# Kernel optimization log

Hardware: AMD Instinct MI355X
Metric: run time of the kernel (lower is better)

The kernel has to match this reference:

```python
import jax, jax.numpy as jnp
import numpy as np

NEG_INF = -1e30


def setup_inputs() -> dict:
    key = jax.random.key(0)
    ks = jax.random.split(key, 7)
    N, C, B = 262144, 256, 8
    feats = jax.random.normal(ks[0], (N, C), dtype=jnp.float32)
    scores = jax.random.normal(ks[1], (N, 1), dtype=jnp.float32)
    w_reg = jax.random.normal(ks[2], (C, 6), dtype=jnp.float32) * 0.01
    w_cls = jax.random.normal(ks[3], (C, 18), dtype=jnp.float32) * 0.01
    b_cls = jax.random.normal(ks[4], (18,), dtype=jnp.float32) * 0.01
    scale = jnp.ones((1,), dtype=jnp.float32)
    batch_ids = jnp.sort(jax.random.randint(ks[5], (N,), 0, B, dtype=jnp.int32))
    return {"feats": feats, "scores": scores, "w_reg": w_reg, "w_cls": w_cls,
            "b_cls": b_cls, "scale": scale, "batch_ids": batch_ids,
            "n_batches": B, "pts_threshold": 8192}


def _prune_mask(scores, batch_ids, n_batches, k):
    # scores: [N,1]; per-batch top-k selection mask (torch.topk + scatter in original).
    s = jax.lax.stop_gradient(scores[:, 0])  # computed under no_grad in torch
    # [B, N]: score where point belongs to batch b, else -inf
    per_batch = jnp.where(batch_ids[None, :] == jnp.arange(n_batches, dtype=batch_ids.dtype)[:, None],
                          s[None, :], NEG_INF)
    kth = jax.lax.top_k(per_batch, k)[0][:, -1]  # [B] k-th largest per cloud
    return s >= kth[batch_ids]  # [N] bool


def reference(feats, scores, w_reg, w_cls, b_cls, scale, batch_ids, n_batches, pts_threshold):
    mask = _prune_mask(scores, batch_ids, n_batches, pts_threshold)
    x = feats * mask[:, None].astype(feats.dtype)  # MinkowskiPruning (fixed-shape: zero out)
    # FCAF3D heads: 1x1 sparse convs == per-point matmuls; reg goes through Scale + exp.
    bbox_pred = jnp.exp(scale[0] * (x @ w_reg))          # [N, 6]
    cls_score = x @ w_cls + b_cls                         # [N, 18]
    return jnp.concatenate([bbox_pred, cls_score], axis=-1)  # [N, 24]
```

## Files before the change

### kernel.cpp

```cpp
#include <hip/hip_runtime.h>
#include <hip/hip_bf16.h>

typedef unsigned int u32;
typedef unsigned short u16;
typedef unsigned long long u64;

#define NBINS 65536
#define MAXB 8

__device__ __forceinline__ u32 mono(float f) {
    u32 u = __float_as_uint(f);
    return (u & 0x80000000u) ? ~u : (u | 0x80000000u);
}

__global__ void k_histA(const float* __restrict__ scores, const int* __restrict__ bids,
                        u32* __restrict__ hist, int N) {
    int i = blockIdx.x * blockDim.x + threadIdx.x;
    if (i >= N) return;
    u32 k = mono(scores[i]) >> 16;
    atomicAdd(&hist[(u32)bids[i] * NBINS + k], 1u);
}

__global__ void k_histB(const float* __restrict__ scores, const int* __restrict__ bids,
                        const u32* __restrict__ Hstar, u32* __restrict__ hist, int N) {
    int i = blockIdx.x * blockDim.x + threadIdx.x;
    if (i >= N) return;
    int b = bids[i];
    u32 key = mono(scores[i]);
    if ((key >> 16) == Hstar[b])
        atomicAdd(&hist[(u32)b * NBINS + (key & 0xFFFFu)], 1u);
}

__device__ int suffix_select(const u32* __restrict__ h, u32 target, u32& remaining_out) {
    __shared__ u32 s[256];
    __shared__ int cc_s;
    __shared__ u32 run_s;
    __shared__ int res_s;
    __shared__ u32 rem_s;
    const int t = threadIdx.x;
    if (t == 0) cc_s = -1;
    u32 tot = 0;
    const uint4* hv = (const uint4*)(h + t * 256);
#pragma unroll 8
    for (int q = 0; q < 64; ++q) { uint4 v = hv[q]; tot += v.x + v.y + v.z + v.w; }
    s[t] = tot;
    __syncthreads();
    for (int off = 1; off < 256; off <<= 1) {
        u32 add = (t + off < 256) ? s[t + off] : 0u;
        __syncthreads();
        s[t] += add;
        __syncthreads();
    }
    u32 nxt = (t == 255) ? 0u : s[t + 1];
    if (s[t] >= target && nxt < target) { cc_s = t; run_s = nxt; }
    __syncthreads();
    int cc = cc_s;
    if (cc < 0) { remaining_out = 0; return -1; }
    u32 running = run_s;
    u32 v = h[cc * 256 + t];
    __syncthreads();
    s[t] = v;
    __syncthreads();
    for (int off = 1; off < 256; off <<= 1) {
        u32 add = (t + off < 256) ? s[t + off] : 0u;
        __syncthreads();
        s[t] += add;
        __syncthreads();
    }
    u32 nxt2 = (t == 255) ? 0u : s[t + 1];
    if (running + s[t] >= target && running + nxt2 < target) {
        res_s = cc * 256 + t;
        rem_s = target - (running + nxt2);
    }
    __syncthreads();
    remaining_out = rem_s;
    return res_s;
}

__global__ void k_scanA(const u32* __restrict__ hist, const int* __restrict__ kptr,
                        u32* __restrict__ Hstar, u32* __restrict__ rB,
                        u32* __restrict__ thresh) {
    int b = blockIdx.x;
    u32 rem;
    int bin = suffix_select(hist + (size_t)b * NBINS, (u32)kptr[0], rem);
    if (threadIdx.x == 0) {
        if (bin < 0) { Hstar[b] = 0xFFFFFFFFu; rB[b] = 0u; thresh[b] = 0u; }
        else { Hstar[b] = (u32)bin; rB[b] = rem; }
    }
}

__global__ void k_scanB(const u32* __restrict__ hist, const u32* __restrict__ Hstar,
                        const u32* __restrict__ rB, u32* __restrict__ thresh) {
    int b = blockIdx.x;
    u32 H = Hstar[b];
    if (H == 0xFFFFFFFFu) return;
    u32 rem;
    int bin = suffix_select(hist + (size_t)b * NBINS, rB[b], rem);
    if (threadIdx.x == 0) thresh[b] = (H << 16) | (u32)bin;
}

__global__ void k_mask(const float* __restrict__ scores, const int* __restrict__ bids,
                       const u32* __restrict__ thresh, const float* __restrict__ bcls,
                       float* __restrict__ out, u32* __restrict__ surv,
                       u32* __restrict__ counter, int N) {
    int i = blockIdx.x * blockDim.x + threadIdx.x;
    bool alive = false;
    if (i < N) alive = mono(scores[i]) >= thresh[bids[i]];
    u64 m = __ballot(alive);
    int lane = threadIdx.x & 63;
    int cnt = __popcll(m);
    if (cnt) {
        u32 base = 0;
        if (lane == 0) base = atomicAdd(counter, (u32)cnt);
        base = (u32)__shfl((int)base, 0, 64);
        if (alive) {
            u32 pos = base + (u32)__popcll(m & ((1ull << lane) - 1ull));
            surv[pos] = (u32)i;
        }
    }
    if (i < N && !alive) {
        __align__(16) float o[24];
#pragma unroll
        for (int j = 0; j < 6; ++j) o[j] = 1.0f;
#pragma unroll
        for (int j = 0; j < 18; ++j) o[6 + j] = bcls[j];
        float4* op = (float4*)(out + (size_t)i * 24);
        const float4* src = (const float4*)o;
#pragma unroll
        for (int q = 0; q < 6; ++q) op[q] = src[q];
    }
}

__global__ __launch_bounds__(256) void k_matmul(
    const float* __restrict__ feats, const float* __restrict__ wreg,
    const float* __restrict__ wcls, const float* __restrict__ bcls,
    const float* __restrict__ scalep, const u32* __restrict__ surv,
    const u32* __restrict__ counter, float* __restrict__ out) {
    const u32 count = counter[0];
    if ((u32)(blockIdx.x * 512) >= count) return;

    __shared__ float W[256 * 24];
    float scl = scalep[0];
    for (int idx = threadIdx.x; idx < 256 * 24; idx += 256) {
        int c = idx / 24, j = idx - c * 24;
        W[idx] = (j < 6) ? scl * wreg[c * 6 + j] : wcls[c * 18 + (j - 6)];
    }
    __syncthreads();

    u32 g = blockIdx.x * 256 + threadIdx.x;
    u32 t0 = 2u * g, t1 = 2u * g + 1u;
    if (t0 >= count) return;
    bool a1 = (t1 < count);
    u32 i0 = surv[t0];
    u32 i1 = a1 ? surv[t1] : i0;
    const float* r0 = feats + (size_t)i0 * 256;
    const float* r1 = feats + (size_t)i1 * 256;

    float acc0[24], acc1[24];
#pragma unroll
    for (int j = 0; j < 24; ++j) { acc0[j] = 0.f; acc1[j] = 0.f; }

    for (int c0 = 0; c0 < 256; c0 += 8) {
        float4 p0a = *(const float4*)(r0 + c0);
        float4 p0b = *(const float4*)(r0 + c0 + 4);
        float4 p1a = *(const float4*)(r1 + c0);
        float4 p1b = *(const float4*)(r1 + c0 + 4);
        float f0[8] = {p0a.x, p0a.y, p0a.z, p0a.w, p0b.x, p0b.y, p0b.z, p0b.w};
        float f1[8] = {p1a.x, p1a.y, p1a.z, p1a.w, p1b.x, p1b.y, p1b.z, p1b.w};
#pragma unroll
        for (int t = 0; t < 8; ++t) {
            const float* wr = &W[(c0 + t) * 24];
#pragma unroll
            for (int j = 0; j < 24; j += 4) {
                float4 w4 = *(const float4*)(wr + j);
                acc0[j + 0] += f0[t] * w4.x;
                acc0[j + 1] += f0[t] * w4.y;
                acc0[j + 2] += f0[t] * w4.z;
                acc0[j + 3] += f0[t] * w4.w;
                acc1[j + 0] += f1[t] * w4.x;
                acc1[j + 1] += f1[t] * w4.y;
                acc1[j + 2] += f1[t] * w4.z;
                acc1[j + 3] += f1[t] * w4.w;
            }
        }
    }

    __align__(16) float o[24];
#pragma unroll
    for (int j = 0; j < 6; ++j) o[j] = __expf(acc0[j]);
#pragma unroll
    for (int j = 0; j < 18; ++j) o[6 + j] = acc0[6 + j] + bcls[j];
    {
        float4* op = (float4*)(out + (size_t)i0 * 24);
        const float4* src = (const float4*)o;
#pragma unroll
        for (int q = 0; q < 6; ++q) op[q] = src[q];
    }
    if (a1) {
#pragma unroll
        for (int j = 0; j < 6; ++j) o[j] = __expf(acc1[j]);
#pragma unroll
        for (int j = 0; j < 18; ++j) o[6 + j] = acc1[6 + j] + bcls[j];
        float4* op = (float4*)(out + (size_t)i1 * 24);
        const float4* src = (const float4*)o;
#pragma unroll
        for (int q = 0; q < 6; ++q) op[q] = src[q];
    }
}

extern "C" void kernel_launch(void* const* d_in, const int* in_sizes, int n_in,
                              void* d_out, int out_size, void* d_ws, size_t ws_size,
                              hipStream_t stream) {
    const float* feats  = (const float*)d_in[0];
    const float* scores = (const float*)d_in[1];
    const float* wreg   = (const float*)d_in[2];
    const float* wcls   = (const float*)d_in[3];
    const float* bcls   = (const float*)d_in[4];
    const float* scalep = (const float*)d_in[5];
    const int*   bids   = (const int*)d_in[6];
    const int*   kptr   = (const int*)d_in[8];
    float* out = (float*)d_out;
    const int N = in_sizes[6];

    u32* counter = (u32*)d_ws;
    u32* hist    = counter + 64;
    u32* thresh  = hist + (size_t)MAXB * NBINS;
    u32* Hstar   = thresh + 16;
    u32* rB      = Hstar + 16;
    u32* surv    = rB + 16;

    size_t zero1 = (64 + (size_t)MAXB * NBINS) * sizeof(u32);
    hipMemsetAsync(d_ws, 0, zero1, stream);

    int nb = (N + 255) / 256;
    k_histA<<<nb, 256, 0, stream>>>(scores, bids, hist, N);
    k_scanA<<<MAXB, 256, 0, stream>>>(hist, kptr, Hstar, rB, thresh);
    hipMemsetAsync(hist, 0, (size_t)MAXB * NBINS * sizeof(u32), stream);
    k_histB<<<nb, 256, 0, stream>>>(scores, bids, Hstar, hist, N);
    k_scanB<<<MAXB, 256, 0, stream>>>(hist, Hstar, rB, thresh);
    k_mask<<<nb, 256, 0, stream>>>(scores, bids, thresh, bcls, out, surv, counter, N);
    k_matmul<<<(N + 511) / 512, 256, 0, stream>>>(feats, wreg, wcls, bcls, scalep, surv, counter, out);
}
```

Before: 490.3 us.

## Fuse mask compaction and matmul into one kernel with block-local survivor lists

```diff
diff --git a/kernel.cpp b/kernel.cpp
--- a/kernel.cpp
+++ b/kernel.cpp
@@ -1,8 +1,6 @@
 #include <hip/hip_runtime.h>
-#include <hip/hip_bf16.h>
 
 typedef unsigned int u32;
-typedef unsigned short u16;
 typedef unsigned long long u64;
 
 #define NBINS 65536
@@ -17,8 +15,7 @@
                         u32* __restrict__ hist, int N) {
     int i = blockIdx.x * blockDim.x + threadIdx.x;
     if (i >= N) return;
-    u32 k = mono(scores[i]) >> 16;
-    atomicAdd(&hist[(u32)bids[i] * NBINS + k], 1u);
+    atomicAdd(&hist[(u32)bids[i] * NBINS + (mono(scores[i]) >> 16)], 1u);
 }
 
 __global__ void k_histB(const float* __restrict__ scores, const int* __restrict__ bids,
@@ -99,112 +96,79 @@
     if (threadIdx.x == 0) thresh[b] = (H << 16) | (u32)bin;
 }
 
-__global__ void k_mask(const float* __restrict__ scores, const int* __restrict__ bids,
-                       const u32* __restrict__ thresh, const float* __restrict__ bcls,
-                       float* __restrict__ out, u32* __restrict__ surv,
-                       u32* __restrict__ counter, int N) {
-    int i = blockIdx.x * blockDim.x + threadIdx.x;
-    bool alive = false;
-    if (i < N) alive = mono(scores[i]) >= thresh[bids[i]];
-    u64 m = __ballot(alive);
-    int lane = threadIdx.x & 63;
-    int cnt = __popcll(m);
-    if (cnt) {
-        u32 base = 0;
-        if (lane == 0) base = atomicAdd(counter, (u32)cnt);
-        base = (u32)__shfl((int)base, 0, 64);
-        if (alive) {
-            u32 pos = base + (u32)__popcll(m & ((1ull << lane) - 1ull));
-            surv[pos] = (u32)i;
-        }
-    }
-    if (i < N && !alive) {
-        __align__(16) float o[24];
-#pragma unroll
-        for (int j = 0; j < 6; ++j) o[j] = 1.0f;
-#pragma unroll
-        for (int j = 0; j < 18; ++j) o[6 + j] = bcls[j];
-        float4* op = (float4*)(out + (size_t)i * 24);
-        const float4* src = (const float4*)o;
-#pragma unroll
-        for (int q = 0; q < 6; ++q) op[q] = src[q];
-    }
-}
-
-__global__ __launch_bounds__(256) void k_matmul(
-    const float* __restrict__ feats, const float* __restrict__ wreg,
-    const float* __restrict__ wcls, const float* __restrict__ bcls,
-    const float* __restrict__ scalep, const u32* __restrict__ surv,
-    const u32* __restrict__ counter, float* __restrict__ out) {
-    const u32 count = counter[0];
-    if ((u32)(blockIdx.x * 512) >= count) return;
+__global__ __launch_bounds__(256) void k_fused(
+    const float* __restrict__ feats, const float* __restrict__ scores,
+    const int* __restrict__ bids, const u32* __restrict__ thresh,
+    const float* __restrict__ wreg, const float* __restrict__ wcls,
+    const float* __restrict__ bcls, const float* __restrict__ scalep,
+    float* __restrict__ out, int N) {
 
     __shared__ float W[256 * 24];
+    __shared__ u32 alive_idx[512];
+    __shared__ u32 nAlive;
+    __shared__ float defrow[24];
+
     float scl = scalep[0];
     for (int idx = threadIdx.x; idx < 256 * 24; idx += 256) {
         int c = idx / 24, j = idx - c * 24;
         W[idx] = (j < 6) ? scl * wreg[c * 6 + j] : wcls[c * 18 + (j - 6)];
     }
-    __syncthreads();
-
-    u32 g = blockIdx.x * 256 + threadIdx.x;
-    u32 t0 = 2u * g, t1 = 2u * g + 1u;
-    if (t0 >= count) return;
-    bool a1 = (t1 < count);
-    u32 i0 = surv[t0];
-    u32 i1 = a1 ? surv[t1] : i0;
-    const float* r0 = feats + (size_t)i0 * 256;
-    const float* r1 = feats + (size_t)i1 * 256;
-
-    float acc0[24], acc1[24];
-#pragma unroll
-    for (int j = 0; j < 24; ++j) { acc0[j] = 0.f; acc1[j] = 0.f; }
-
-    for (int c0 = 0; c0 < 256; c0 += 8) {
-        float4 p0a = *(const float4*)(r0 + c0);
-        float4 p0b = *(const float4*)(r0 + c0 + 4);
-        float4 p1a = *(const float4*)(r1 + c0);
-        float4 p1b = *(const float4*)(r1 + c0 + 4);
-        float f0[8] = {p0a.x, p0a.y, p0a.z, p0a.w, p0b.x, p0b.y, p0b.z, p0b.w};
-        float f1[8] = {p1a.x, p1a.y, p1a.z, p1a.w, p1b.x, p1b.y, p1b.z, p1b.w};
-#pragma unroll
-        for (int t = 0; t < 8; ++t) {
-            const float* wr = &W[(c0 + t) * 24];
-#pragma unroll
-            for (int j = 0; j < 24; j += 4) {
-                float4 w4 = *(const float4*)(wr + j);
-                acc0[j + 0] += f0[t] * w4.x;
-                acc0[j + 1] += f0[t] * w4.y;
-                acc0[j + 2] += f0[t] * w4.z;
-                acc0[j + 3] += f0[t] * w4.w;
-                acc1[j + 0] += f1[t] * w4.x;
-                acc1[j + 1] += f1[t] * w4.y;
-                acc1[j + 2] += f1[t] * w4.z;
-                acc1[j + 3] += f1[t] * w4.w;
+    if (threadIdx.x == 0) nAlive = 0;
+    if (threadIdx.x < 24) defrow[threadIdx.x] = (threadIdx.x < 6) ? 1.0f : bcls[threadIdx.x - 6];
+    __syncthreads();
+
+    const int base = blockIdx.x * 512;
+#pragma unroll
+    for (int q = 0; q < 2; ++q) {
+        int i = base + threadIdx.x + q * 256;
+        if (i < N) {
+            bool alive = mono(scores[i]) >= thresh[bids[i]];
+            if (alive) {
+                u32 p = atomicAdd(&nAlive, 1u);
+                alive_idx[p] = (u32)i;
+            } else {
+                float4* op = (float4*)(out + (size_t)i * 24);
+                const float4* s4 = (const float4*)defrow;
+#pragma unroll
+                for (int w = 0; w < 6; ++w) op[w] = s4[w];
             }
         }
     }
-
-    __align__(16) float o[24];
-#pragma unroll
-    for (int j = 0; j < 6; ++j) o[j] = __expf(acc0[j]);
-#pragma unroll
-    for (int j = 0; j < 18; ++j) o[6 + j] = acc0[6 + j] + bcls[j];
-    {
-        float4* op = (float4*)(out + (size_t)i0 * 24);
-        const float4* src = (const float4*)o;
-#pragma unroll
-        for (int q = 0; q < 6; ++q) op[q] = src[q];
-    }
-    if (a1) {
-#pragma unroll
-        for (int j = 0; j < 6; ++j) o[j] = __expf(acc1[j]);
-#pragma unroll
-        for (int j = 0; j < 18; ++j) o[6 + j] = acc1[6 + j] + bcls[j];
-        float4* op = (float4*)(out + (size_t)i1 * 24);
-        const float4* src = (const float4*)o;
-#pragma unroll
-        for (int q = 0; q < 6; ++q) op[q] = src[q];
+    __syncthreads();
+    const u32 cnt = nAlive;
+
+    for (u32 r = threadIdx.x; r < cnt; r += 256) {
+        u32 i = alive_idx[r];
+        const float* row = feats + (size_t)i * 256;
+        float acc[24];
+#pragma unroll
+        for (int j = 0; j < 24; ++j) acc[j] = 0.f;
+        for (int c0 = 0; c0 < 256; c0 += 8) {
+            float4 a = *(const float4*)(row + c0);
+            float4 b = *(const float4*)(row + c0 + 4);
+            float f[8] = {a.x, a.y, a.z, a.w, b.x, b.y, b.z, b.w};
+#pragma unroll
+            for (int t = 0; t < 8; ++t) {
+                const float* wr = &W[(c0 + t) * 24];
+#pragma unroll
+                for (int j = 0; j < 24; j += 4) {
+                    float4 w4 = *(const float4*)(wr + j);
+                    acc[j + 0] += f[t] * w4.x;
+                    acc[j + 1] += f[t] * w4.y;
+                    acc[j + 2] += f[t] * w4.z;
+                    acc[j + 3] += f[t] * w4.w;
+                }
+            }
+        }
+        __align__(16) float o[24];
+#pragma unroll
+        for (int j = 0; j < 6; ++j) o[j] = __expf(acc[j]);
+#pragma unroll
+        for (int j = 0; j < 18; ++j) o[6 + j] = acc[6 + j] + defrow[6 + j];
+        float4* op = (float4*)(out + (size_t)i * 24);
+        const float4* s4 = (const float4*)o;
+#pragma unroll
+        for (int w = 0; w < 6; ++w) op[w] = s4[w];
     }
 }
 
@@ -222,22 +186,19 @@
     float* out = (float*)d_out;
     const int N = in_sizes[6];
 
-    u32* counter = (u32*)d_ws;
-    u32* hist    = counter + 64;
-    u32* thresh  = hist + (size_t)MAXB * NBINS;
-    u32* Hstar   = thresh + 16;
-    u32* rB      = Hstar + 16;
-    u32* surv    = rB + 16;
-
-    size_t zero1 = (64 + (size_t)MAXB * NBINS) * sizeof(u32);
-    hipMemsetAsync(d_ws, 0, zero1, stream);
+    u32* histA  = (u32*)d_ws;
+    u32* histB  = histA + (size_t)MAXB * NBINS;
+    u32* thresh = histB + (size_t)MAXB * NBINS;
+    u32* Hstar  = thresh + 16;
+    u32* rB     = Hstar + 16;
+
+    hipMemsetAsync(d_ws, 0, (2 * (size_t)MAXB * NBINS) * sizeof(u32), stream);
 
     int nb = (N + 255) / 256;
-    k_histA<<<nb, 256, 0, stream>>>(scores, bids, hist, N);
-    k_scanA<<<MAXB, 256, 0, stream>>>(hist, kptr, Hstar, rB, thresh);
-    hipMemsetAsync(hist, 0, (size_t)MAXB * NBINS * sizeof(u32), stream);
-    k_histB<<<nb, 256, 0, stream>>>(scores, bids, Hstar, hist, N);
-    k_scanB<<<MAXB, 256, 0, stream>>>(hist, Hstar, rB, thresh);
-    k_mask<<<nb, 256, 0, stream>>>(scores, bids, thresh, bcls, out, surv, counter, N);
-    k_matmul<<<(N + 511) / 512, 256, 0, stream>>>(feats, wreg, wcls, bcls, scalep, surv, counter, out);
-}
+    k_histA<<<nb, 256, 0, stream>>>(scores, bids, histA, N);
+    k_scanA<<<MAXB, 256, 0, stream>>>(histA, kptr, Hstar, rB, thresh);
+    k_histB<<<nb, 256, 0, stream>>>(scores, bids, Hstar, histB, N);
+    k_scanB<<<MAXB, 256, 0, stream>>>(histB, Hstar, rB, thresh);
+    k_fused<<<(N + 511) / 512, 256, 0, stream>>>(feats, scores, bids, thresh,
+                                                 wreg, wcls, bcls, scalep, out, N);
+}
```

After: 414.6 us. 15.4% less time.
